# Kernel tuning notes

Hardware: AMD Instinct MI355X
Metric: run time of the kernel (lower is better)

## Reference

```python
import jax, jax.numpy as jnp
import numpy as np

N = 4096          # number of real POIs (distance_matrix is [N, N])
D = 64            # poi_dim
B = 8             # users (samples)
DAYS = 4          # days per user
L = 64            # POI ids per day
SCALE = 50.0      # max distance -> arange(0, 50+0.5, 0.5) = 101 bucket boundaries
NUM_INTERVALS = 101


def setup_inputs() -> dict:
    key = jax.random.key(0)
    k1, k2, k3 = jax.random.split(key, 3)
    poi_weight = jax.random.normal(k1, (N + 1, D), dtype=jnp.float32)
    distance_matrix = jax.random.uniform(k2, (N, N), dtype=jnp.float32) * SCALE
    # POI ids in [1, N]: no padding zeros, so lastDay[lastDay != 0] == lastDay (static shape)
    seqInDay = jax.random.randint(k3, (B * DAYS, L), 1, N + 1)
    sampleIdOfDay_set = jnp.repeat(jnp.arange(B), DAYS)
    return {
        "poi_weight": poi_weight,
        "distance_matrix": distance_matrix,
        "seqInDay": seqInDay,
        "sampleIdOfDay_set": sampleIdOfDay_set,
        "GCN_layer_num": 2,
    }


def reference(poi_weight, distance_matrix, seqInDay, sampleIdOfDay_set, GCN_layer_num):
    # group days by sample id (stable sort == torch sorted+groupby); equal group sizes
    ids = np.asarray(sampleIdOfDay_set)
    order = np.argsort(ids, kind="stable")
    nb = int(np.unique(ids).size)
    days = ids.shape[0] // nb
    samples = seqInDay[order].reshape(nb, days, -1)            # [B, days, L]

    poi_emb = poi_weight[1:]                                    # [N, D]
    intervals = jnp.arange(0.0, SCALE + 0.5, 0.5)               # [NUM_INTERVALS]
    # bucket of every distance entry under the torch mask rule:
    # intervals[i-1] <= d < intervals[i]  <=>  searchsorted(side='right')
    dm_bucket = jnp.searchsorted(intervals, distance_matrix, side="right")  # [N, N] int
    diag = jnp.arange(distance_matrix.shape[0])
    scale = jnp.sqrt(jnp.float32(poi_weight.shape[1]))

    def per_sample(sample):                                     # sample: [days, L]
        lastDay = sample[-1]                                    # all ids nonzero
        spans = distance_matrix[lastDay[:-1] - 1, lastDay[1:] - 1]
        # torch.bucketize(right=False) == searchsorted side='left'
        span_idx = jnp.searchsorted(intervals, spans, side="left")
        w = jnp.bincount(span_idx, length=NUM_INTERVALS).astype(jnp.float32)
        w = w / w.sum()
        # buckets actually visited by this sample (torch loops over unique())
        present = jnp.zeros(NUM_INTERVALS, dtype=bool).at[span_idx].set(True)
        W = jnp.where(present[dm_bucket], w[dm_bucket], 0.0)    # [N, N]
        W = W.at[diag, diag].set(1.0)                            # fill_diagonal_(1)
        deg = jnp.maximum(jnp.sqrt(W.sum(-1, keepdims=True)), 1e-12)
        adj = W / deg / deg.T                                    # D^-1/2 A D^-1/2
        out = poi_emb
        layer = poi_emb
        for _ in range(GCN_layer_num):
            layer = jnp.tanh(adj @ layer)
            out = out + layer                                    # sum over stacked layers
        table = jnp.concatenate([poi_weight[:1], out], axis=0)  # [N+1, D]
        return table[sample] * scale                             # [days, L, D]

    res = jax.vmap(per_sample)(samples)                          # [B, days, L, D]
    return res.reshape(nb * days, samples.shape[-1], -1)
```

## Files before the change

### kernel.cpp

```cpp
#include <hip/hip_runtime.h>
#include <hip/hip_bf16.h>
#include <math.h>

typedef __bf16 bf16x8 __attribute__((ext_vector_type(8)));
typedef float  f32x4  __attribute__((ext_vector_type(4)));
typedef unsigned short ushort_t;
typedef unsigned char  u8;
typedef unsigned int   u32;

#define N_POI 4096
#define NB    8
#define NDAYS 4
#define LSEQ  64
#define NROWS 32
#define NBINS 102
#define KC    3

static __device__ __forceinline__ u32 bf16bits(float f) {
  u32 x = __float_as_uint(f);
  return ((x + 0x7FFFu + ((x >> 16) & 1u)) >> 16) & 0xFFFFu;
}

static __device__ __forceinline__ float b2f(ushort_t u) {
  return __uint_as_float((u32)u << 16);
}

static __device__ __forceinline__ void gload16(void* lds, const void* g) {
  __builtin_amdgcn_global_load_lds(
      (const __attribute__((address_space(1))) u32*)g,
      (__attribute__((address_space(3))) u32*)lds, 16, 0, 0);
}

__global__ __launch_bounds__(64) void k_sample(const int* __restrict__ ids,
                                               const int* __restrict__ seq,
                                               const float* __restrict__ dm,
                                               float* __restrict__ tfp,
                                               u32* __restrict__ tbu,
                                               int* __restrict__ meta) {
  __shared__ int sh_ids[NROWS];
  __shared__ int sh_order[NROWS];
  __shared__ int sh_cnt[NBINS];
  __shared__ int sh_last[LSEQ];
  __shared__ int sh_nb;
  const int tid = threadIdx.x, s = blockIdx.x;
  if (tid < NROWS) sh_ids[tid] = ids[tid];
  for (int k = tid; k < NBINS; k += 64) sh_cnt[k] = 0;
  if (tid == 0) sh_nb = 0;
  __syncthreads();
  if (tid < NROWS) {
    const int my = sh_ids[tid];
    int rank = 0, first = 1;
    for (int j = 0; j < NROWS; ++j) {
      const int v = sh_ids[j];
      if (v < my || (v == my && j < tid)) rank++;
      if (v == my && j < tid) first = 0;
    }
    sh_order[rank] = tid;
    if (first) atomicAdd(&sh_nb, 1);
  }
  __syncthreads();
  const int nb = sh_nb;
  const int days = NROWS / nb;
  if (s == 0) {
    if (tid < NROWS) meta[tid] = sh_order[tid];
    if (tid == 0) meta[NROWS] = days;
  }
  const int lastRow = sh_order[s * days + days - 1];
  sh_last[tid] = seq[lastRow * LSEQ + tid];
  __syncthreads();
  if (tid < LSEQ - 1) {
    const float v = dm[(size_t)(sh_last[tid] - 1) * N_POI + (sh_last[tid + 1] - 1)];
    int si = (int)ceilf(2.0f * v);
    si = min(max(si, 0), 101);
    atomicAdd(&sh_cnt[si], 1);
  }
  __syncthreads();
  const float inv = 1.0f / (float)(LSEQ - 1);
  for (int k = tid; k < 128; k += 64) {
    const float wv = (k < NBINS) ? (float)sh_cnt[k] * inv : 0.0f;
    tfp[s * 128 + k] = wv;
    tbu[s * 128 + k] = bf16bits(wv);
  }
}

__global__ __launch_bounds__(256) void k_bucket(const float* __restrict__ dm,
                                                const float* __restrict__ tfp,
                                                u8* __restrict__ bucket,
                                                float* __restrict__ rbuf) {
  const int row = blockIdx.x, tid = threadIdx.x;
  __shared__ int h[2][NBINS];
  __shared__ float tl[NB][NBINS];
  __shared__ int sh_bii;
  for (int k = tid; k < 2 * NBINS; k += 256) ((int*)h)[k] = 0;
  __syncthreads();
  const float4* drow = (const float4*)(dm + (size_t)row * N_POI);
  u32* brow = (u32*)(bucket + (size_t)row * N_POI);
  int* hp = h[tid >> 7];
  const int jdiag = row >> 2;
  for (int it = 0; it < 4; ++it) {
    const int j = it * 256 + tid;
    const float4 v = drow[j];
    const int b0 = min((int)(2.0f * v.x) + 1, 101);
    const int b1 = min((int)(2.0f * v.y) + 1, 101);
    const int b2 = min((int)(2.0f * v.z) + 1, 101);
    const int b3 = min((int)(2.0f * v.w) + 1, 101);
    atomicAdd(&hp[b0], 1); atomicAdd(&hp[b1], 1);
    atomicAdd(&hp[b2], 1); atomicAdd(&hp[b3], 1);
    const u32 pk = (u32)b0 | ((u32)b1 << 8) | ((u32)b2 << 16) | ((u32)b3 << 24);
    if (j == jdiag) sh_bii = (int)((pk >> (8 * (row & 3))) & 255u);
    brow[j] = pk;
  }
  for (int idx = tid; idx < NB * NBINS; idx += 256)
    tl[idx / NBINS][idx % NBINS] = tfp[(idx / NBINS) * 128 + (idx % NBINS)];
  __syncthreads();
  for (int k = tid; k < NBINS; k += 256) h[0][k] += h[1][k];
  __syncthreads();
  const int s = tid >> 5, ln = tid & 31;
  float dot = 0.f;
  for (int k = ln; k < NBINS; k += 32) dot += (float)h[0][k] * tl[s][k];
#pragma unroll
  for (int off = 16; off >= 1; off >>= 1) dot += __shfl_down(dot, off, 32);
  if (ln == 0) {
    const float ri = rsqrtf(dot - tl[s][sh_bii] + 1.0f);
    rbuf[s * N_POI + row] = ri;
  }
}

__global__ __launch_bounds__(256) void k_rows(const float* __restrict__ rbuf,
                                              const float* __restrict__ poi,
                                              ushort_t* __restrict__ y1t) {
  const int s = blockIdx.y;
  const int i = blockIdx.x * 256 + threadIdx.x;
  const float ri = rbuf[s * N_POI + i];
#pragma unroll 8
  for (int d = 0; d < 64; ++d) {
    const float pv = poi[(size_t)(i + 1) * 64 + d];
    y1t[((size_t)s * 64 + d) * N_POI + i] = (ushort_t)bf16bits(ri * pv);
  }
}

__global__ __launch_bounds__(256, 3) void k_layer(
    const u8* __restrict__ bucket, const u32* __restrict__ tbu,
    const ushort_t* __restrict__ yin, ushort_t* __restrict__ part) {
  const int rb = blockIdx.x, kc = blockIdx.y, s = blockIdx.z;
  const int tid = threadIdx.x;
  const int lane = tid & 63, w = tid >> 6;
  const int loff = tid & 31;

  __shared__ u32 trep[NBINS * 32];
  __shared__ ushort_t Ybuf[2][64 * 64];

  const int gi0 = rb * 128;
  const int r0 = gi0 + w * 32 + (lane & 15);
  const u8* brow0 = bucket + (size_t)r0 * N_POI;
  const u8* brow1 = brow0 + (size_t)16 * N_POI;
  const int kq = (lane >> 4) * 8;

  const ushort_t* ybase = yin + (size_t)s * 64 * N_POI;

  const int d0s = tid >> 3, d1s = 32 + d0s;
  const int bly = (tid & 7) * 16;
  const int sw0 = bly ^ (((d0s & 7) ^ ((d0s >> 3) & 1)) << 4);
  const int sw1 = bly ^ (((d1s & 7) ^ ((d1s >> 3) & 1)) << 4);
  const char* gsrc0 = (const char*)(ybase + (size_t)d0s * N_POI) + sw0;
  const char* gsrc1 = (const char*)(ybase + (size_t)d1s * N_POI) + sw1;

  const int kt0 = (kc * 64) / KC, kt1 = ((kc + 1) * 64) / KC;

  uint2 bpA[4], bpB[4];

#define LOADB_(dst, ktv)                                   \
  {                                                        \
    const int _kb = (ktv) * 64;                            \
    dst[0] = *(const uint2*)(brow0 + _kb + kq);            \
    dst[1] = *(const uint2*)(brow0 + _kb + 32 + kq);       \
    dst[2] = *(const uint2*)(brow1 + _kb + kq);            \
    dst[3] = *(const uint2*)(brow1 + _kb + 32 + kq);       \
  }

#define STAGE_(bufi, ktv)                                  \
  {                                                        \
    const size_t _kb = (size_t)(ktv) * 128;                \
    char* _lb = (char*)&Ybuf[bufi][0] + tid * 16;          \
    gload16(_lb, gsrc0 + _kb);                             \
    gload16(_lb + 4096, gsrc1 + _kb);                      \
  }

  STAGE_(0, kt0);
  LOADB_(bpA, kt0);
  for (int idx = tid; idx < NBINS * 32; idx += 256)
    trep[idx] = tbu[s * 128 + (idx >> 5)];

  f32x4 acc[2][4];
#pragma unroll
  for (int mt = 0; mt < 2; ++mt)
#pragma unroll
    for (int nt = 0; nt < 4; ++nt) acc[mt][nt] = (f32x4){0.f, 0.f, 0.f, 0.f};

  asm volatile("s_waitcnt vmcnt(0)" ::: "memory");
  __syncthreads();

#define BODY_(CB, PB, CUR)                                                     \
  {                                                                            \
    const int k0 = kt * 64;                                                    \
    if (kt + 1 < kt1) { STAGE_((CUR) ^ 1, kt + 1); LOADB_(PB, kt + 1); }       \
    bf16x8 afr[2][2];                                                          \
    _Pragma("unroll") for (int mt = 0; mt < 2; ++mt) {                         \
      _Pragma("unroll") for (int ks = 0; ks < 2; ++ks) {                       \
        const uint2 bb = CB[mt * 2 + ks];                                      \
        u32 tv[8];                                                             \
        _Pragma("unroll") for (int e = 0; e < 4; ++e) tv[e] =                  \
            trep[((bb.x >> (8 * e)) & 255u) * 32 + loff];                      \
        _Pragma("unroll") for (int e = 0; e < 4; ++e) tv[4 + e] =              \
            trep[((bb.y >> (8 * e)) & 255u) * 32 + loff];                      \
        const u32 de = (u32)(r0 + mt * 16 - (k0 + ks * 32 + kq));              \
        if (de < 8u) {                              \
          _Pragma("unroll") for (int e = 0; e < 8; ++e)                        \
              if (de == (u32)e) tv[e] = 0x3F80u;                               \
        }                                                                      \
        uint4 pk;                                                              \
        pk.x = tv[0] | (tv[1] << 16);                                          \
        pk.y = tv[2] | (tv[3] << 16);                                          \
        pk.z = tv[4] | (tv[5] << 16);                                          \
        pk.w = tv[6] | (tv[7] << 16);                                          \
        union { uint4 u; bf16x8 v; } cvt;                                      \
        cvt.u = pk;                                                            \
        afr[mt][ks] = cvt.v;                                                   \
      }                                                                        \
    }                                                                          \
    const char* _yb = (const char*)&Ybuf[CUR][0];                              \
    _Pragma("unroll") for (int ks = 0; ks < 2; ++ks) {                         \
      _Pragma("unroll") for (int nt = 0; nt < 4; ++nt) {                       \
        const int rY = nt * 16 + (lane & 15);                                  \
        const int pm = (rY & 7) ^ ((rY >> 3) & 1);                             \
        const int la = rY * 128 + (((ks * 4 + (lane >> 4)) ^ pm) << 4);        \
        union { uint4 u; bf16x8 v; } bu;                                       \
        bu.u = *(const uint4*)(_yb + la);                                      \
        acc[0][nt] = __builtin_amdgcn_mfma_f32_16x16x32_bf16(afr[0][ks], bu.v, \
                                                             acc[0][nt], 0, 0, 0); \
        acc[1][nt] = __builtin_amdgcn_mfma_f32_16x16x32_bf16(afr[1][ks], bu.v, \
                                                             acc[1][nt], 0, 0, 0); \
      }                                                                        \
    }                                                                          \
    asm volatile("s_waitcnt vmcnt(0)" ::: "memory");                           \
    __syncthreads();      \
  }

  int kt = kt0;
  while (true) {
    BODY_(bpA, bpB, 0);
    if (++kt >= kt1) break;
    BODY_(bpB, bpA, 1);
    if (++kt >= kt1) break;
  }

#undef BODY_
#undef STAGE_
#undef LOADB_

#pragma unroll
  for (int mt = 0; mt < 2; ++mt) {
#pragma unroll
    for (int e = 0; e < 4; ++e) {
      const int row = gi0 + w * 32 + mt * 16 + (lane >> 4) * 4 + e;
#pragma unroll
      for (int nt = 0; nt < 4; ++nt) {
        const int col = nt * 16 + (lane & 15);
        part[(((size_t)kc * NB + s) * N_POI + row) * 64 + col] =
            (ushort_t)bf16bits(acc[mt][nt][e]);
      }
    }
  }
}

__global__ __launch_bounds__(256) void k_reduce(
    const ushort_t* __restrict__ part, const float* __restrict__ rbuf,
    const float* __restrict__ poi, float* __restrict__ table,
    ushort_t* __restrict__ y2t) {
  const int it = blockIdx.x, s = blockIdx.y, tid = threadIdx.x;
  __shared__ ushort_t Tt[64 * 72];
#pragma unroll
  for (int j = 0; j < 2; ++j) {
    const int s2 = tid + j * 256;
    const int iloc = s2 >> 3, d0 = (s2 & 7) * 8;
    const int i = it * 64 + iloc;
    const size_t po = ((size_t)s * N_POI + i) * 64 + d0;
    uint4 p0 = *(const uint4*)(part + po);
    uint4 p1 = *(const uint4*)(part + (size_t)NB * N_POI * 64 + po);
    uint4 p2 = *(const uint4*)(part + (size_t)2 * NB * N_POI * 64 + po);
    const u32* a0 = (const u32*)&p0;
    const u32* a1 = (const u32*)&p1;
    const u32* a2 = (const u32*)&p2;
    float x[8];
#pragma unroll
    for (int q = 0; q < 4; ++q) {
      x[2 * q]     = __uint_as_float(a0[q] << 16) + __uint_as_float(a1[q] << 16) +
                     __uint_as_float(a2[q] << 16);
      x[2 * q + 1] = __uint_as_float(a0[q] & 0xFFFF0000u) +
                     __uint_as_float(a1[q] & 0xFFFF0000u) +
                     __uint_as_float(a2[q] & 0xFFFF0000u);
    }
    const float ri = rbuf[s * N_POI + i];
    float t[8];
#pragma unroll
    for (int e = 0; e < 8; ++e) t[e] = tanhf(ri * x[e]);
    float* trow = table + po;
    const float* prow = poi + (size_t)(i + 1) * 64 + d0;
    float4 pz0 = *(const float4*)prow;
    float4 pz1 = *(const float4*)(prow + 4);
    float4 o0 = {pz0.x + t[0], pz0.y + t[1], pz0.z + t[2], pz0.w + t[3]};
    float4 o1 = {pz1.x + t[4], pz1.y + t[5], pz1.z + t[6], pz1.w + t[7]};
    *(float4*)trow = o0;
    *(float4*)(trow + 4) = o1;
#pragma unroll
    for (int e = 0; e < 8; ++e)
      Tt[(d0 + e) * 72 + iloc] = (ushort_t)bf16bits(ri * t[e]);
  }
  __syncthreads();
  const int d = tid >> 2, i0 = (tid & 3) * 16;
  uint4 a = *(const uint4*)&Tt[d * 72 + i0];
  uint4 b = *(const uint4*)&Tt[d * 72 + i0 + 8];
  ushort_t* dst = y2t + ((size_t)s * 64 + d) * N_POI + it * 64 + i0;
  *(uint4*)dst = a;
  *(uint4*)(dst + 8) = b;
}

__global__ __launch_bounds__(256) void k_gather(const int* __restrict__ seq,
                                                const int* __restrict__ meta,
                                                const float* __restrict__ table,
                                                const float* __restrict__ poi,
                                                const ushort_t* __restrict__ part,
                                                const float* __restrict__ rbuf,
                                                float* __restrict__ out) {
  const int r = blockIdx.x;
  const int p = blockIdx.y * 4 + (threadIdx.x >> 6);
  const int d = threadIdx.x & 63;
  const int days = meta[NROWS];
  const int srcrow = meta[r];
  const int g = r / days;
  const int id = seq[srcrow * LSEQ + p];
  float v;
  if (id == 0) {
    v = poi[d];
  } else {
    const size_t po = ((size_t)g * N_POI + (id - 1)) * 64 + d;
    const float x2 = b2f(part[po]) +
                     b2f(part[(size_t)NB * N_POI * 64 + po]) +
                     b2f(part[(size_t)2 * NB * N_POI * 64 + po]);
    v = table[po] + tanhf(rbuf[g * N_POI + (id - 1)] * x2);
  }
  out[((size_t)r * LSEQ + p) * 64 + d] = v * 8.0f;
}

extern "C" void kernel_launch(void* const* d_in, const int* in_sizes, int n_in,
                              void* d_out, int out_size, void* d_ws, size_t ws_size,
                              hipStream_t stream) {
  (void)in_sizes; (void)n_in; (void)out_size; (void)ws_size;
  const float* poi = (const float*)d_in[0];
  const float* dm  = (const float*)d_in[1];
  const int*   seq = (const int*)d_in[2];
  const int*   ids = (const int*)d_in[3];

  char* ws = (char*)d_ws;
  size_t off = 0;
  auto carve = [&](size_t bytes) {
    char* p = ws + off;
    off += (bytes + 255) & ~(size_t)255;
    return p;
  };
  u8*       bucket = (u8*)carve((size_t)N_POI * N_POI);
  float*    tfp    = (float*)carve((size_t)NB * 128 * 4);
  u32*      tbu    = (u32*)carve((size_t)NB * 128 * 4);
  float*    rbuf   = (float*)carve((size_t)NB * N_POI * 4);
  float*    table  = (float*)carve((size_t)NB * N_POI * 64 * 4);
  ushort_t* y1t    = (ushort_t*)table;
  ushort_t* y2t    = (ushort_t*)carve((size_t)NB * 64 * N_POI * 2);
  ushort_t* part   = (ushort_t*)carve((size_t)KC * NB * N_POI * 64 * 2);
  int*      meta   = (int*)carve(256);

  k_sample<<<NB, 64, 0, stream>>>(ids, seq, dm, tfp, tbu, meta);
  k_bucket<<<N_POI, 256, 0, stream>>>(dm, tfp, bucket, rbuf);
  k_rows<<<dim3(16, NB), 256, 0, stream>>>(rbuf, poi, y1t);
  k_layer<<<dim3(32, KC, NB), 256, 0, stream>>>(bucket, tbu, y1t, part);
  k_reduce<<<dim3(64, NB), 256, 0, stream>>>(part, rbuf, poi, table, y2t);
  k_layer<<<dim3(32, KC, NB), 256, 0, stream>>>(bucket, tbu, y2t, part);
  k_gather<<<dim3(NROWS, 16), 256, 0, stream>>>(seq, meta, table, poi, part, rbuf,
                                                (float*)d_out);
}
```

Measured before the change: 206.3 us.

## Process two samples per layer block sharing bucket loads and LDS lookups

Each k_layer block now handles two samples at once. The bucket byte tile and the lookup table are loaded once, with both samples' bf16 weights packed into one 32-bit LDS entry, so the per-byte gather serves two MFMA A-fragments. To keep the grid size the same, the K split is raised from 3 to 6, and the reduce and gather kernels now sum a variable number of partial buffers. The cost is twice the accumulator registers, a larger LDS Y buffer and double the partial-sum write and read traffic.

```diff
diff --git a/kernel.cpp b/kernel.cpp
--- a/kernel.cpp
+++ b/kernel.cpp
@@ -14,7 +14,7 @@
 #define LSEQ  64
 #define NROWS 32
 #define NBINS 102
-#define KC    3
+#define KC    6
 
 static __device__ __forceinline__ u32 bf16bits(float f) {
   u32 x = __float_as_uint(f);
@@ -142,13 +142,14 @@
 __global__ __launch_bounds__(256, 3) void k_layer(
     const u8* __restrict__ bucket, const u32* __restrict__ tbu,
     const ushort_t* __restrict__ yin, ushort_t* __restrict__ part) {
-  const int rb = blockIdx.x, kc = blockIdx.y, s = blockIdx.z;
+  const int rb = blockIdx.x, kc = blockIdx.y, g = blockIdx.z;
+  const int s0 = 2 * g, s1 = 2 * g + 1;
   const int tid = threadIdx.x;
   const int lane = tid & 63, w = tid >> 6;
   const int loff = tid & 31;
 
   __shared__ u32 trep[NBINS * 32];
-  __shared__ ushort_t Ybuf[2][64 * 64];
+  __shared__ ushort_t Ybuf[2][2][64 * 64];
 
   const int gi0 = rb * 128;
   const int r0 = gi0 + w * 32 + (lane & 15);
@@ -156,14 +157,17 @@
   const u8* brow1 = brow0 + (size_t)16 * N_POI;
   const int kq = (lane >> 4) * 8;
 
-  const ushort_t* ybase = yin + (size_t)s * 64 * N_POI;
+  const ushort_t* ybase0 = yin + (size_t)s0 * 64 * N_POI;
+  const ushort_t* ybase1 = yin + (size_t)s1 * 64 * N_POI;
 
   const int d0s = tid >> 3, d1s = 32 + d0s;
   const int bly = (tid & 7) * 16;
   const int sw0 = bly ^ (((d0s & 7) ^ ((d0s >> 3) & 1)) << 4);
   const int sw1 = bly ^ (((d1s & 7) ^ ((d1s >> 3) & 1)) << 4);
-  const char* gsrc0 = (const char*)(ybase + (size_t)d0s * N_POI) + sw0;
-  const char* gsrc1 = (const char*)(ybase + (size_t)d1s * N_POI) + sw1;
+  const char* g00 = (const char*)(ybase0 + (size_t)d0s * N_POI) + sw0;
+  const char* g01 = (const char*)(ybase0 + (size_t)d1s * N_POI) + sw1;
+  const char* g10 = (const char*)(ybase1 + (size_t)d0s * N_POI) + sw0;
+  const char* g11 = (const char*)(ybase1 + (size_t)d1s * N_POI) + sw1;
 
   const int kt0 = (kc * 64) / KC, kt1 = ((kc + 1) * 64) / KC;
 
@@ -181,21 +185,28 @@
 #define STAGE_(bufi, ktv)                                  \
   {                                                        \
     const size_t _kb = (size_t)(ktv) * 128;                \
-    char* _lb = (char*)&Ybuf[bufi][0] + tid * 16;          \
-    gload16(_lb, gsrc0 + _kb);                             \
-    gload16(_lb + 4096, gsrc1 + _kb);                      \
+    char* _lb = (char*)&Ybuf[bufi][0][0] + tid * 16;       \
+    gload16(_lb, g00 + _kb);                               \
+    gload16(_lb + 4096, g01 + _kb);                        \
+    gload16(_lb + 8192, g10 + _kb);                        \
+    gload16(_lb + 12288, g11 + _kb);                       \
   }
 
   STAGE_(0, kt0);
   LOADB_(bpA, kt0);
-  for (int idx = tid; idx < NBINS * 32; idx += 256)
-    trep[idx] = tbu[s * 128 + (idx >> 5)];
-
-  f32x4 acc[2][4];
+  for (int idx = tid; idx < NBINS * 32; idx += 256) {
+    const int b = idx >> 5;
+    trep[idx] = tbu[s0 * 128 + b] | (tbu[s1 * 128 + b] << 16);
+  }
+
+  f32x4 acc0[2][4], acc1[2][4];
 #pragma unroll
   for (int mt = 0; mt < 2; ++mt)
 #pragma unroll
-    for (int nt = 0; nt < 4; ++nt) acc[mt][nt] = (f32x4){0.f, 0.f, 0.f, 0.f};
+    for (int nt = 0; nt < 4; ++nt) {
+      acc0[mt][nt] = (f32x4){0.f, 0.f, 0.f, 0.f};
+      acc1[mt][nt] = (f32x4){0.f, 0.f, 0.f, 0.f};
+    }
 
   asm volatile("s_waitcnt vmcnt(0)" ::: "memory");
   __syncthreads();
@@ -204,7 +215,7 @@
   {                                                                            \
     const int k0 = kt * 64;                                                    \
     if (kt + 1 < kt1) { STAGE_((CUR) ^ 1, kt + 1); LOADB_(PB, kt + 1); }       \
-    bf16x8 afr[2][2];                                                          \
+    bf16x8 af0[2][2], af1[2][2];                                               \
     _Pragma("unroll") for (int mt = 0; mt < 2; ++mt) {                         \
       _Pragma("unroll") for (int ks = 0; ks < 2; ++ks) {                       \
         const uint2 bb = CB[mt * 2 + ks];                                      \
@@ -214,32 +225,42 @@
         _Pragma("unroll") for (int e = 0; e < 4; ++e) tv[4 + e] =              \
             trep[((bb.y >> (8 * e)) & 255u) * 32 + loff];                      \
         const u32 de = (u32)(r0 + mt * 16 - (k0 + ks * 32 + kq));              \
-        if (de < 8u) {                              \
+        if (de < 8u) {             \
           _Pragma("unroll") for (int e = 0; e < 8; ++e)                        \
-              if (de == (u32)e) tv[e] = 0x3F80u;                               \
+              if (de == (u32)e) tv[e] = 0x3F803F80u;                           \
         }                                                                      \
-        uint4 pk;                                                              \
-        pk.x = tv[0] | (tv[1] << 16);                                          \
-        pk.y = tv[2] | (tv[3] << 16);                                          \
-        pk.z = tv[4] | (tv[5] << 16);                                          \
-        pk.w = tv[6] | (tv[7] << 16);                                          \
-        union { uint4 u; bf16x8 v; } cvt;                                      \
-        cvt.u = pk;                                                            \
-        afr[mt][ks] = cvt.v;                                                   \
+        uint4 p0, p1;                                                          \
+        p0.x = (tv[0] & 0xFFFFu) | (tv[1] << 16);                              \
+        p0.y = (tv[2] & 0xFFFFu) | (tv[3] << 16);                              \
+        p0.z = (tv[4] & 0xFFFFu) | (tv[5] << 16);                              \
+        p0.w = (tv[6] & 0xFFFFu) | (tv[7] << 16);                              \
+        p1.x = (tv[0] >> 16) | (tv[1] & 0xFFFF0000u);                          \
+        p1.y = (tv[2] >> 16) | (tv[3] & 0xFFFF0000u);                          \
+        p1.z = (tv[4] >> 16) | (tv[5] & 0xFFFF0000u);                          \
+        p1.w = (tv[6] >> 16) | (tv[7] & 0xFFFF0000u);                          \
+        union { uint4 u; bf16x8 v; } c0, c1;                                   \
+        c0.u = p0; c1.u = p1;                                                  \
+        af0[mt][ks] = c0.v; af1[mt][ks] = c1.v;                                \
       }                                                                        \
     }                                                                          \
-    const char* _yb = (const char*)&Ybuf[CUR][0];                              \
+    const char* _y0 = (const char*)&Ybuf[CUR][0][0];                           \
+    const char* _y1 = (const char*)&Ybuf[CUR][1][0];                           \
     _Pragma("unroll") for (int ks = 0; ks < 2; ++ks) {                         \
       _Pragma("unroll") for (int nt = 0; nt < 4; ++nt) {                       \
         const int rY = nt * 16 + (lane & 15);                                  \
         const int pm = (rY & 7) ^ ((rY >> 3) & 1);                             \
         const int la = rY * 128 + (((ks * 4 + (lane >> 4)) ^ pm) << 4);        \
-        union { uint4 u; bf16x8 v; } bu;                                       \
-        bu.u = *(const uint4*)(_yb + la);                                      \
-        acc[0][nt] = __builtin_amdgcn_mfma_f32_16x16x32_bf16(afr[0][ks], bu.v, \
-                                                             acc[0][nt], 0, 0, 0); \
-        acc[1][nt] = __builtin_amdgcn_mfma_f32_16x16x32_bf16(afr[1][ks], bu.v, \
-                                                             acc[1][nt], 0, 0, 0); \
+        union { uint4 u; bf16x8 v; } b0, b1;                                   \
+        b0.u = *(const uint4*)(_y0 + la);                                      \
+        b1.u = *(const uint4*)(_y1 + la);                                      \
+        acc0[0][nt] = __builtin_amdgcn_mfma_f32_16x16x32_bf16(af0[0][ks], b0.v, \
+                                                              acc0[0][nt], 0, 0, 0); \
+        acc0[1][nt] = __builtin_amdgcn_mfma_f32_16x16x32_bf16(af0[1][ks], b0.v, \
+                                                              acc0[1][nt], 0, 0, 0); \
+        acc1[0][nt] = __builtin_amdgcn_mfma_f32_16x16x32_bf16(af1[0][ks], b1.v, \
+                                                              acc1[0][nt], 0, 0, 0); \
+        acc1[1][nt] = __builtin_amdgcn_mfma_f32_16x16x32_bf16(af1[1][ks], b1.v, \
+                                                              acc1[1][nt], 0, 0, 0); \
       }                                                                        \
     }                                                                          \
     asm volatile("s_waitcnt vmcnt(0)" ::: "memory");                           \
@@ -266,8 +287,10 @@
 #pragma unroll
       for (int nt = 0; nt < 4; ++nt) {
         const int col = nt * 16 + (lane & 15);
-        part[(((size_t)kc * NB + s) * N_POI + row) * 64 + col] =
-            (ushort_t)bf16bits(acc[mt][nt][e]);
+        part[(((size_t)kc * NB + s0) * N_POI + row) * 64 + col] =
+            (ushort_t)bf16bits(acc0[mt][nt][e]);
+        part[(((size_t)kc * NB + s1) * N_POI + row) * 64 + col] =
+            (ushort_t)bf16bits(acc1[mt][nt][e]);
       }
     }
   }
@@ -285,20 +308,16 @@
     const int iloc = s2 >> 3, d0 = (s2 & 7) * 8;
     const int i = it * 64 + iloc;
     const size_t po = ((size_t)s * N_POI + i) * 64 + d0;
-    uint4 p0 = *(const uint4*)(part + po);
-    uint4 p1 = *(const uint4*)(part + (size_t)NB * N_POI * 64 + po);
-    uint4 p2 = *(const uint4*)(part + (size_t)2 * NB * N_POI * 64 + po);
-    const u32* a0 = (const u32*)&p0;
-    const u32* a1 = (const u32*)&p1;
-    const u32* a2 = (const u32*)&p2;
-    float x[8];
-#pragma unroll
-    for (int q = 0; q < 4; ++q) {
-      x[2 * q]     = __uint_as_float(a0[q] << 16) + __uint_as_float(a1[q] << 16) +
-                     __uint_as_float(a2[q] << 16);
-      x[2 * q + 1] = __uint_as_float(a0[q] & 0xFFFF0000u) +
-                     __uint_as_float(a1[q] & 0xFFFF0000u) +
-                     __uint_as_float(a2[q] & 0xFFFF0000u);
+    float x[8] = {0.f, 0.f, 0.f, 0.f, 0.f, 0.f, 0.f, 0.f};
+#pragma unroll
+    for (int c = 0; c < KC; ++c) {
+      uint4 p = *(const uint4*)(part + (size_t)c * NB * N_POI * 64 + po);
+      const u32* a = (const u32*)&p;
+#pragma unroll
+      for (int q = 0; q < 4; ++q) {
+        x[2 * q]     += __uint_as_float(a[q] << 16);
+        x[2 * q + 1] += __uint_as_float(a[q] & 0xFFFF0000u);
+      }
     }
     const float ri = rbuf[s * N_POI + i];
     float t[8];
@@ -344,9 +363,10 @@
     v = poi[d];
   } else {
     const size_t po = ((size_t)g * N_POI + (id - 1)) * 64 + d;
-    const float x2 = b2f(part[po]) +
-                     b2f(part[(size_t)NB * N_POI * 64 + po]) +
-                     b2f(part[(size_t)2 * NB * N_POI * 64 + po]);
+    float x2 = 0.f;
+#pragma unroll
+    for (int c = 0; c < KC; ++c)
+      x2 += b2f(part[(size_t)c * NB * N_POI * 64 + po]);
     v = table[po] + tanhf(rbuf[g * N_POI + (id - 1)] * x2);
   }
   out[((size_t)r * LSEQ + p) * 64 + d] = v * 8.0f;
@@ -381,9 +401,9 @@
   k_sample<<<NB, 64, 0, stream>>>(ids, seq, dm, tfp, tbu, meta);
   k_bucket<<<N_POI, 256, 0, stream>>>(dm, tfp, bucket, rbuf);
   k_rows<<<dim3(16, NB), 256, 0, stream>>>(rbuf, poi, y1t);
-  k_layer<<<dim3(32, KC, NB), 256, 0, stream>>>(bucket, tbu, y1t, part);
+  k_layer<<<dim3(32, KC, 4), 256, 0, stream>>>(bucket, tbu, y1t, part);
   k_reduce<<<dim3(64, NB), 256, 0, stream>>>(part, rbuf, poi, table, y2t);
-  k_layer<<<dim3(32, KC, NB), 256, 0, stream>>>(bucket, tbu, y2t, part);
+  k_layer<<<dim3(32, KC, 4), 256, 0, stream>>>(bucket, tbu, y2t, part);
   k_gather<<<dim3(NROWS, 16), 256, 0, stream>>>(seq, meta, table, poi, part, rbuf,
                                                 (float*)d_out);
 }
```

Result: faster. 185.2 us (-10.2%).

## Compute second GCN layer only for gathered rows and load Y directly into registers

Applied to the files above, without the earlier changes.

The second layer's adjacency-times-features product is now computed only for the 2048 POI rows that the final gather actually reads, selected through a new rowids table built in k_sample, instead of for all 4096 rows per sample. That layer splits K into 16 chunks with fp32 partial outputs, which k_gather sums. The first-layer kernel now loads Y fragments straight from global memory into registers with inline asm instead of staging through LDS. It also spreads the bucket histogram across four copies and vectorises the poi loads in k_rows. The trade-offs are more partial-sum traffic in the gather and possibly uncoalesced Y loads in layer one.

```diff
diff --git a/kernel.cpp b/kernel.cpp
--- a/kernel.cpp
+++ b/kernel.cpp
@@ -4,6 +4,8 @@
 
 typedef __bf16 bf16x8 __attribute__((ext_vector_type(8)));
 typedef float  f32x4  __attribute__((ext_vector_type(4)));
+typedef unsigned int u32x4 __attribute__((ext_vector_type(4)));
+typedef unsigned int u32x2 __attribute__((ext_vector_type(2)));
 typedef unsigned short ushort_t;
 typedef unsigned char  u8;
 typedef unsigned int   u32;
@@ -15,14 +17,19 @@
 #define NROWS 32
 #define NBINS 102
 #define KC    3
+#define KC2   16
+#define NPOS  2048
 
 static __device__ __forceinline__ u32 bf16bits(float f) {
   u32 x = __float_as_uint(f);
   return ((x + 0x7FFFu + ((x >> 16) & 1u)) >> 16) & 0xFFFFu;
 }
 
-static __device__ __forceinline__ float b2f(ushort_t u) {
-  return __uint_as_float((u32)u << 16);
+static __device__ __forceinline__ float lo16f(u32 v) {
+  return __uint_as_float(v << 16);
+}
+static __device__ __forceinline__ float hi16f(u32 v) {
+  return __uint_as_float(v & 0xFFFF0000u);
 }
 
 static __device__ __forceinline__ void gload16(void* lds, const void* g) {
@@ -36,7 +43,8 @@
                                                const float* __restrict__ dm,
                                                float* __restrict__ tfp,
                                                u32* __restrict__ tbu,
-                                               int* __restrict__ meta) {
+                                               int* __restrict__ meta,
+                                               int* __restrict__ rowids) {
   __shared__ int sh_ids[NROWS];
   __shared__ int sh_order[NROWS];
   __shared__ int sh_cnt[NBINS];
@@ -65,6 +73,11 @@
     if (tid < NROWS) meta[tid] = sh_order[tid];
     if (tid == 0) meta[NROWS] = days;
   }
+  for (int day = 0; day < days; ++day) {
+    const int r = s * days + day;
+    const int src = sh_order[r];
+    rowids[r * LSEQ + tid] = max(seq[src * LSEQ + tid] - 1, 0);
+  }
   const int lastRow = sh_order[s * days + days - 1];
   sh_last[tid] = seq[lastRow * LSEQ + tid];
   __syncthreads();
@@ -88,14 +101,14 @@
                                                 u8* __restrict__ bucket,
                                                 float* __restrict__ rbuf) {
   const int row = blockIdx.x, tid = threadIdx.x;
-  __shared__ int h[2][NBINS];
+  __shared__ int h[4][NBINS];
   __shared__ float tl[NB][NBINS];
   __shared__ int sh_bii;
-  for (int k = tid; k < 2 * NBINS; k += 256) ((int*)h)[k] = 0;
+  for (int k = tid; k < 4 * NBINS; k += 256) ((int*)h)[k] = 0;
   __syncthreads();
   const float4* drow = (const float4*)(dm + (size_t)row * N_POI);
   u32* brow = (u32*)(bucket + (size_t)row * N_POI);
-  int* hp = h[tid >> 7];
+  int* hp = h[tid >> 6];
   const int jdiag = row >> 2;
   for (int it = 0; it < 4; ++it) {
     const int j = it * 256 + tid;
@@ -113,7 +126,8 @@
   for (int idx = tid; idx < NB * NBINS; idx += 256)
     tl[idx / NBINS][idx % NBINS] = tfp[(idx / NBINS) * 128 + (idx % NBINS)];
   __syncthreads();
-  for (int k = tid; k < NBINS; k += 256) h[0][k] += h[1][k];
+  for (int k = tid; k < NBINS; k += 256)
+    h[0][k] += h[1][k] + h[2][k] + h[3][k];
   __syncthreads();
   const int s = tid >> 5, ln = tid & 31;
   float dot = 0.f;
@@ -132,10 +146,15 @@
   const int s = blockIdx.y;
   const int i = blockIdx.x * 256 + threadIdx.x;
   const float ri = rbuf[s * N_POI + i];
-#pragma unroll 8
-  for (int d = 0; d < 64; ++d) {
-    const float pv = poi[(size_t)(i + 1) * 64 + d];
-    y1t[((size_t)s * 64 + d) * N_POI + i] = (ushort_t)bf16bits(ri * pv);
+  const float4* prow = (const float4*)(poi + (size_t)(i + 1) * 64);
+  ushort_t* dst = y1t + (size_t)s * 64 * N_POI + i;
+#pragma unroll
+  for (int q = 0; q < 16; ++q) {
+    const float4 v = prow[q];
+    dst[(size_t)(4 * q + 0) * N_POI] = (ushort_t)bf16bits(ri * v.x);
+    dst[(size_t)(4 * q + 1) * N_POI] = (ushort_t)bf16bits(ri * v.y);
+    dst[(size_t)(4 * q + 2) * N_POI] = (ushort_t)bf16bits(ri * v.z);
+    dst[(size_t)(4 * q + 3) * N_POI] = (ushort_t)bf16bits(ri * v.w);
   }
 }
 
@@ -148,7 +167,6 @@
   const int loff = tid & 31;
 
   __shared__ u32 trep[NBINS * 32];
-  __shared__ ushort_t Ybuf[2][64 * 64];
 
   const int gi0 = rb * 128;
   const int r0 = gi0 + w * 32 + (lane & 15);
@@ -156,8 +174,188 @@
   const u8* brow1 = brow0 + (size_t)16 * N_POI;
   const int kq = (lane >> 4) * 8;
 
+  const ushort_t* yr0 =
+      yin + (size_t)s * 64 * N_POI + (size_t)(lane & 15) * N_POI + kq;
+
+  const int kt0 = (kc * 64) / KC, kt1 = ((kc + 1) * 64) / KC;
+
+  u32x4 ybA[8], ybB[8];
+  u32x2 bpA[4], bpB[4];
+
+#define LOADY_ASM(dst, ktv)                                                    \
+  {                                                                            \
+    const int _ky = (ktv) * 64;                                                \
+    _Pragma("unroll") for (int ks = 0; ks < 2; ++ks)                           \
+        _Pragma("unroll") for (int nt = 0; nt < 4; ++nt)                       \
+            asm volatile("global_load_dwordx4 %0, %1, off"                     \
+                         : "=v"(dst[ks * 4 + nt])                              \
+                         : "v"(yr0 + (size_t)nt * 16 * N_POI + _ky + ks * 32)); \
+  }
+
+#define LOADB_ASM(dst, ktv)                                                    \
+  {                                                                            \
+    const int _kb = (ktv) * 64;                                                \
+    asm volatile("global_load_dwordx2 %0, %1, off"                             \
+                 : "=v"(dst[0]) : "v"(brow0 + _kb + kq));                      \
+    asm volatile("global_load_dwordx2 %0, %1, off"                             \
+                 : "=v"(dst[1]) : "v"(brow0 + _kb + 32 + kq));                 \
+    asm volatile("global_load_dwordx2 %0, %1, off"                             \
+                 : "=v"(dst[2]) : "v"(brow1 + _kb + kq));                      \
+    asm volatile("global_load_dwordx2 %0, %1, off"                             \
+                 : "=v"(dst[3]) : "v"(brow1 + _kb + 32 + kq));                 \
+  }
+
+  LOADY_ASM(ybA, kt0);
+  LOADB_ASM(bpA, kt0);
+  for (int idx = tid; idx < NBINS * 32; idx += 256)
+    trep[idx] = tbu[s * 128 + (idx >> 5)];
+
+  f32x4 acc[2][4];
+#pragma unroll
+  for (int mt = 0; mt < 2; ++mt)
+#pragma unroll
+    for (int nt = 0; nt < 4; ++nt) acc[mt][nt] = (f32x4){0.f, 0.f, 0.f, 0.f};
+
+  __syncthreads();
+
+#define BODY_(CY, CB, PY, PB)                                                  \
+  {                                                                            \
+    asm volatile("s_waitcnt vmcnt(0)" ::: "memory");                           \
+    __builtin_amdgcn_sched_barrier(0);                                         \
+    if (kt + 1 < kt1) { LOADY_ASM(PY, kt + 1); LOADB_ASM(PB, kt + 1); }        \
+    const int k0 = kt * 64;                                                    \
+    bf16x8 afr[2][2];                                                          \
+    _Pragma("unroll") for (int mt = 0; mt < 2; ++mt) {                         \
+      _Pragma("unroll") for (int ks = 0; ks < 2; ++ks) {                       \
+        const u32x2 bb = CB[mt * 2 + ks];                                      \
+        u32 tv[8];                                                             \
+        _Pragma("unroll") for (int e = 0; e < 4; ++e) tv[e] =                  \
+            trep[((bb[0] >> (8 * e)) & 255u) * 32 + loff];                     \
+        _Pragma("unroll") for (int e = 0; e < 4; ++e) tv[4 + e] =              \
+            trep[((bb[1] >> (8 * e)) & 255u) * 32 + loff];                     \
+        const u32 de = (u32)(r0 + mt * 16 - (k0 + ks * 32 + kq));              \
+        if (de < 8u) {                              \
+          _Pragma("unroll") for (int e = 0; e < 8; ++e)                        \
+              if (de == (u32)e) tv[e] = 0x3F80u;                               \
+        }                                                                      \
+        uint4 pk;                                                              \
+        pk.x = tv[0] | (tv[1] << 16);                                          \
+        pk.y = tv[2] | (tv[3] << 16);                                          \
+        pk.z = tv[4] | (tv[5] << 16);                                          \
+        pk.w = tv[6] | (tv[7] << 16);                                          \
+        union { uint4 u; bf16x8 v; } cvt;                                      \
+        cvt.u = pk;                                                            \
+        afr[mt][ks] = cvt.v;                                                   \
+      }                                                                        \
+    }                                                                          \
+    _Pragma("unroll") for (int ks = 0; ks < 2; ++ks) {                         \
+      _Pragma("unroll") for (int nt = 0; nt < 4; ++nt) {                       \
+        union { u32x4 u; bf16x8 v; } bu;                                       \
+        bu.u = CY[ks * 4 + nt];                                                \
+        acc[0][nt] = __builtin_amdgcn_mfma_f32_16x16x32_bf16(afr[0][ks], bu.v, \
+                                                             acc[0][nt], 0, 0, 0); \
+        acc[1][nt] = __builtin_amdgcn_mfma_f32_16x16x32_bf16(afr[1][ks], bu.v, \
+                                                             acc[1][nt], 0, 0, 0); \
+      }                                                                        \
+    }                                                                          \
+  }
+
+  int kt = kt0;
+  while (true) {
+    BODY_(ybA, bpA, ybB, bpB);
+    if (++kt >= kt1) break;
+    BODY_(ybB, bpB, ybA, bpA);
+    if (++kt >= kt1) break;
+  }
+
+#undef BODY_
+#undef LOADY_ASM
+#undef LOADB_ASM
+
+#pragma unroll
+  for (int mt = 0; mt < 2; ++mt) {
+#pragma unroll
+    for (int e = 0; e < 4; ++e) {
+      const int row = gi0 + w * 32 + mt * 16 + (lane >> 4) * 4 + e;
+#pragma unroll
+      for (int nt = 0; nt < 4; ++nt) {
+        const int col = nt * 16 + (lane & 15);
+        part[(((size_t)kc * NB + s) * N_POI + row) * 64 + col] =
+            (ushort_t)bf16bits(acc[mt][nt][e]);
+      }
+    }
+  }
+}
+
+__global__ __launch_bounds__(256) void k_reduce(
+    const ushort_t* __restrict__ part, const float* __restrict__ rbuf,
+    const float* __restrict__ poi, float* __restrict__ table,
+    ushort_t* __restrict__ y2t) {
+  const int it = blockIdx.x, s = blockIdx.y, tid = threadIdx.x;
+  __shared__ ushort_t Tt[64 * 72];
+#pragma unroll
+  for (int j = 0; j < 2; ++j) {
+    const int s2 = tid + j * 256;
+    const int iloc = s2 >> 3, d0 = (s2 & 7) * 8;
+    const int i = it * 64 + iloc;
+    const size_t po = ((size_t)s * N_POI + i) * 64 + d0;
+    float x[8] = {0.f, 0.f, 0.f, 0.f, 0.f, 0.f, 0.f, 0.f};
+#pragma unroll
+    for (int c = 0; c < KC; ++c) {
+      uint4 p = *(const uint4*)(part + (size_t)c * NB * N_POI * 64 + po);
+      const u32* a = (const u32*)&p;
+#pragma unroll
+      for (int q = 0; q < 4; ++q) {
+        x[2 * q]     += lo16f(a[q]);
+        x[2 * q + 1] += hi16f(a[q]);
+      }
+    }
+    const float ri = rbuf[s * N_POI + i];
+    float t[8];
+#pragma unroll
+    for (int e = 0; e < 8; ++e) t[e] = tanhf(ri * x[e]);
+    float* trow = table + po;
+    const float* prow = poi + (size_t)(i + 1) * 64 + d0;
+    float4 pz0 = *(const float4*)prow;
+    float4 pz1 = *(const float4*)(prow + 4);
+    float4 o0 = {pz0.x + t[0], pz0.y + t[1], pz0.z + t[2], pz0.w + t[3]};
+    float4 o1 = {pz1.x + t[4], pz1.y + t[5], pz1.z + t[6], pz1.w + t[7]};
+    *(float4*)trow = o0;
+    *(float4*)(trow + 4) = o1;
+#pragma unroll
+    for (int e = 0; e < 8; ++e)
+      Tt[(d0 + e) * 72 + iloc] = (ushort_t)bf16bits(ri * t[e]);
+  }
+  __syncthreads();
+  const int d = tid >> 2, i0 = (tid & 3) * 16;
+  uint4 a = *(const uint4*)&Tt[d * 72 + i0];
+  uint4 b = *(const uint4*)&Tt[d * 72 + i0 + 8];
+  ushort_t* dst = y2t + ((size_t)s * 64 + d) * N_POI + it * 64 + i0;
+  *(uint4*)dst = a;
+  *(uint4*)(dst + 8) = b;
+}
+
+__global__ __launch_bounds__(256) void k_layer2(
+    const u8* __restrict__ bucket, const u32* __restrict__ tbu,
+    const ushort_t* __restrict__ yin, const int* __restrict__ rowids,
+    float* __restrict__ part2) {
+  const int rb = blockIdx.x, kc = blockIdx.y;
+  const int s = rb >> 1;
+  const int tid = threadIdx.x;
+  const int lane = tid & 63, w = tid >> 6;
+  const int loff = tid & 31;
+
+  __shared__ u32 trep[NBINS * 32];
+  __shared__ ushort_t Ybuf[2][64 * 64];
+
+  const int pos0 = rb * 128 + w * 32 + (lane & 15);
+  const int rid0 = rowids[pos0];
+  const int rid1 = rowids[pos0 + 16];
+  const u8* brow0 = bucket + (size_t)rid0 * N_POI;
+  const u8* brow1 = bucket + (size_t)rid1 * N_POI;
+  const int kq = (lane >> 4) * 8;
+
   const ushort_t* ybase = yin + (size_t)s * 64 * N_POI;
-
   const int d0s = tid >> 3, d1s = 32 + d0s;
   const int bly = (tid & 7) * 16;
   const int sw0 = bly ^ (((d0s & 7) ^ ((d0s >> 3) & 1)) << 4);
@@ -165,7 +363,7 @@
   const char* gsrc0 = (const char*)(ybase + (size_t)d0s * N_POI) + sw0;
   const char* gsrc1 = (const char*)(ybase + (size_t)d1s * N_POI) + sw1;
 
-  const int kt0 = (kc * 64) / KC, kt1 = ((kc + 1) * 64) / KC;
+  const int kt0 = kc * 4, kt1 = kt0 + 4;
 
   uint2 bpA[4], bpB[4];
 
@@ -213,7 +411,8 @@
             trep[((bb.x >> (8 * e)) & 255u) * 32 + loff];                      \
         _Pragma("unroll") for (int e = 0; e < 4; ++e) tv[4 + e] =              \
             trep[((bb.y >> (8 * e)) & 255u) * 32 + loff];                      \
-        const u32 de = (u32)(r0 + mt * 16 - (k0 + ks * 32 + kq));              \
+        const int grow = mt ? rid1 : rid0;                                     \
+        const u32 de = (u32)(grow - (k0 + ks * 32 + kq));                      \
         if (de < 8u) {                              \
           _Pragma("unroll") for (int e = 0; e < 8; ++e)                        \
               if (de == (u32)e) tv[e] = 0x3F80u;                               \
@@ -243,7 +442,7 @@
       }                                                                        \
     }                                                                          \
     asm volatile("s_waitcnt vmcnt(0)" ::: "memory");                           \
-    __syncthreads();      \
+    __syncthreads();                                                           \
   }
 
   int kt = kt0;
@@ -262,74 +461,21 @@
   for (int mt = 0; mt < 2; ++mt) {
 #pragma unroll
     for (int e = 0; e < 4; ++e) {
-      const int row = gi0 + w * 32 + mt * 16 + (lane >> 4) * 4 + e;
+      const int pos = rb * 128 + w * 32 + mt * 16 + (lane >> 4) * 4 + e;
 #pragma unroll
       for (int nt = 0; nt < 4; ++nt) {
         const int col = nt * 16 + (lane & 15);
-        part[(((size_t)kc * NB + s) * N_POI + row) * 64 + col] =
-            (ushort_t)bf16bits(acc[mt][nt][e]);
+        part2[((size_t)kc * NPOS + pos) * 64 + col] = acc[mt][nt][e];
       }
     }
   }
-}
-
-__global__ __launch_bounds__(256) void k_reduce(
-    const ushort_t* __restrict__ part, const float* __restrict__ rbuf,
-    const float* __restrict__ poi, float* __restrict__ table,
-    ushort_t* __restrict__ y2t) {
-  const int it = blockIdx.x, s = blockIdx.y, tid = threadIdx.x;
-  __shared__ ushort_t Tt[64 * 72];
-#pragma unroll
-  for (int j = 0; j < 2; ++j) {
-    const int s2 = tid + j * 256;
-    const int iloc = s2 >> 3, d0 = (s2 & 7) * 8;
-    const int i = it * 64 + iloc;
-    const size_t po = ((size_t)s * N_POI + i) * 64 + d0;
-    uint4 p0 = *(const uint4*)(part + po);
-    uint4 p1 = *(const uint4*)(part + (size_t)NB * N_POI * 64 + po);
-    uint4 p2 = *(const uint4*)(part + (size_t)2 * NB * N_POI * 64 + po);
-    const u32* a0 = (const u32*)&p0;
-    const u32* a1 = (const u32*)&p1;
-    const u32* a2 = (const u32*)&p2;
-    float x[8];
-#pragma unroll
-    for (int q = 0; q < 4; ++q) {
-      x[2 * q]     = __uint_as_float(a0[q] << 16) + __uint_as_float(a1[q] << 16) +
-                     __uint_as_float(a2[q] << 16);
-      x[2 * q + 1] = __uint_as_float(a0[q] & 0xFFFF0000u) +
-                     __uint_as_float(a1[q] & 0xFFFF0000u) +
-                     __uint_as_float(a2[q] & 0xFFFF0000u);
-    }
-    const float ri = rbuf[s * N_POI + i];
-    float t[8];
-#pragma unroll
-    for (int e = 0; e < 8; ++e) t[e] = tanhf(ri * x[e]);
-    float* trow = table + po;
-    const float* prow = poi + (size_t)(i + 1) * 64 + d0;
-    float4 pz0 = *(const float4*)prow;
-    float4 pz1 = *(const float4*)(prow + 4);
-    float4 o0 = {pz0.x + t[0], pz0.y + t[1], pz0.z + t[2], pz0.w + t[3]};
-    float4 o1 = {pz1.x + t[4], pz1.y + t[5], pz1.z + t[6], pz1.w + t[7]};
-    *(float4*)trow = o0;
-    *(float4*)(trow + 4) = o1;
-#pragma unroll
-    for (int e = 0; e < 8; ++e)
-      Tt[(d0 + e) * 72 + iloc] = (ushort_t)bf16bits(ri * t[e]);
-  }
-  __syncthreads();
-  const int d = tid >> 2, i0 = (tid & 3) * 16;
-  uint4 a = *(const uint4*)&Tt[d * 72 + i0];
-  uint4 b = *(const uint4*)&Tt[d * 72 + i0 + 8];
-  ushort_t* dst = y2t + ((size_t)s * 64 + d) * N_POI + it * 64 + i0;
-  *(uint4*)dst = a;
-  *(uint4*)(dst + 8) = b;
 }
 
 __global__ __launch_bounds__(256) void k_gather(const int* __restrict__ seq,
                                                 const int* __restrict__ meta,
                                                 const float* __restrict__ table,
                                                 const float* __restrict__ poi,
-                                                const ushort_t* __restrict__ part,
+                                                const float* __restrict__ part2,
                                                 const float* __restrict__ rbuf,
                                                 float* __restrict__ out) {
   const int r = blockIdx.x;
@@ -337,17 +483,19 @@
   const int d = threadIdx.x & 63;
   const int days = meta[NROWS];
   const int srcrow = meta[r];
-  const int g = r / days;
+  const int s = r / days;
   const int id = seq[srcrow * LSEQ + p];
   float v;
   if (id == 0) {
     v = poi[d];
   } else {
-    const size_t po = ((size_t)g * N_POI + (id - 1)) * 64 + d;
-    const float x2 = b2f(part[po]) +
-                     b2f(part[(size_t)NB * N_POI * 64 + po]) +
-                     b2f(part[(size_t)2 * NB * N_POI * 64 + po]);
-    v = table[po] + tanhf(rbuf[g * N_POI + (id - 1)] * x2);
+    const size_t gq = (size_t)r * LSEQ + p;
+    float x2 = 0.f;
+#pragma unroll
+    for (int c = 0; c < KC2; ++c)
+      x2 += part2[((size_t)c * NPOS + gq) * 64 + d];
+    v = table[((size_t)s * N_POI + (id - 1)) * 64 + d] +
+        tanhf(rbuf[s * N_POI + (id - 1)] * x2);
   }
   out[((size_t)r * LSEQ + p) * 64 + d] = v * 8.0f;
 }
@@ -376,14 +524,16 @@
   ushort_t* y1t    = (ushort_t*)table;
   ushort_t* y2t    = (ushort_t*)carve((size_t)NB * 64 * N_POI * 2);
   ushort_t* part   = (ushort_t*)carve((size_t)KC * NB * N_POI * 64 * 2);
+  float*    part2  = (float*)carve((size_t)KC2 * NPOS * 64 * 4);
+  int*      rowids = (int*)carve((size_t)NPOS * 4);
   int*      meta   = (int*)carve(256);
 
-  k_sample<<<NB, 64, 0, stream>>>(ids, seq, dm, tfp, tbu, meta);
+  k_sample<<<NB, 64, 0, stream>>>(ids, seq, dm, tfp, tbu, meta, rowids);
   k_bucket<<<N_POI, 256, 0, stream>>>(dm, tfp, bucket, rbuf);
   k_rows<<<dim3(16, NB), 256, 0, stream>>>(rbuf, poi, y1t);
   k_layer<<<dim3(32, KC, NB), 256, 0, stream>>>(bucket, tbu, y1t, part);
   k_reduce<<<dim3(64, NB), 256, 0, stream>>>(part, rbuf, poi, table, y2t);
-  k_layer<<<dim3(32, KC, NB), 256, 0, stream>>>(bucket, tbu, y2t, part);
-  k_gather<<<dim3(NROWS, 16), 256, 0, stream>>>(seq, meta, table, poi, part, rbuf,
+  k_layer2<<<dim3(16, KC2), 256, 0, stream>>>(bucket, tbu, y2t, rowids, part2);
+  k_gather<<<dim3(NROWS, 16), 256, 0, stream>>>(seq, meta, table, poi, part2, rbuf,
                                                 (float*)d_out);
 }
```

New measurement: 227.3 us. 10.2% more time.
